# Performance work log

Hardware: AMD Instinct MI355X
Metric: run time of the kernel (lower is better)

## Reference

```python
import jax, jax.numpy as jnp
import numpy as np

B, N, S, D = 8, 325, 64, 256
H = 8
HD = D // H  # head_dim = 32


def setup_inputs() -> dict:
    key = jax.random.key(0)
    ks = jax.random.split(key, 5)
    x = jax.random.normal(ks[0], (B, N, S, D), dtype=jnp.float32)
    # nn.Linear params: weight [out, in], bias [out]
    w_qkv = jax.random.normal(ks[1], (3 * D, D), dtype=jnp.float32) * (1.0 / np.sqrt(D))
    b_qkv = jax.random.normal(ks[2], (3 * D,), dtype=jnp.float32) * 0.01
    w_proj = jax.random.normal(ks[3], (D, D), dtype=jnp.float32) * (1.0 / np.sqrt(D))
    b_proj = jax.random.normal(ks[4], (D,), dtype=jnp.float32) * 0.01
    return {"x": x, "w_qkv": w_qkv, "b_qkv": b_qkv, "w_proj": w_proj, "b_proj": b_proj}


def reference(x, w_qkv, b_qkv, w_proj, b_proj):
    b, n, s, d = x.shape
    scale = (d // H) ** -0.5
    xf = x.reshape(b * n, s, d)                              # [BN, S, D]
    qkv = jnp.einsum('bsd,ed->bse', xf, w_qkv) + b_qkv       # [BN, S, 3D]
    qkv = qkv.reshape(b * n, s, 3, H, HD)
    qkv = jnp.transpose(qkv, (2, 0, 3, 1, 4))                # [3, BN, H, S, HD]
    q, k, v = qkv[0], qkv[1], qkv[2]
    attn = jnp.einsum('bhqe,bhke->bhqk', q, k) * scale       # [BN, H, S, S]
    attn = jax.nn.softmax(attn, axis=-1)
    out = jnp.einsum('bhqk,bhke->bhqe', attn, v)             # [BN, H, S, HD]
    out = jnp.transpose(out, (0, 2, 1, 3)).reshape(b * n, s, d)
    out = jnp.einsum('bsd,ed->bse', out, w_proj) + b_proj
    return out.reshape(b, n, s, d)
```

## Files before the change

kernel.cpp:

```cpp
#include <hip/hip_runtime.h>
#include <hip/hip_bf16.h>


namespace {

constexpr int S_LEN = 64;
constexpr int DM    = 256;
constexpr int SD    = S_LEN * DM;
constexpr int NQKV  = 3 * DM * DM;

typedef float f32x4 __attribute__((ext_vector_type(4)));
typedef short s16x8 __attribute__((ext_vector_type(8)));

union BF2 { __hip_bfloat162 h; unsigned u; };
__device__ __forceinline__ unsigned pkbf2(float a, float b) {
  float2 t; t.x = a; t.y = b;
  BF2 cv; cv.h = __float22bfloat162_rn(t);
  return cv.u;
}

__device__ __forceinline__ s16x8 xpose_frag(f32x4 a0, f32x4 a1, int c, int g) {
  const int src0 = ((g & 1) << 5) + c;
  const int src1 = src0 + 16;
  unsigned p00 = pkbf2(a0[0], a0[1]);
  unsigned p01 = pkbf2(a0[2], a0[3]);
  unsigned p10 = pkbf2(a1[0], a1[1]);
  unsigned p11 = pkbf2(a1[2], a1[3]);
  const bool hi = (g & 2) != 0;
  unsigned w0a = (unsigned)__shfl((int)p00, src0);
  unsigned w0b = (unsigned)__shfl((int)p10, src0);
  unsigned w1a = (unsigned)__shfl((int)p01, src0);
  unsigned w1b = (unsigned)__shfl((int)p11, src0);
  unsigned w2a = (unsigned)__shfl((int)p00, src1);
  unsigned w2b = (unsigned)__shfl((int)p10, src1);
  unsigned w3a = (unsigned)__shfl((int)p01, src1);
  unsigned w3b = (unsigned)__shfl((int)p11, src1);
  union { s16x8 v; unsigned u[4]; } r;
  r.u[0] = hi ? w0b : w0a;
  r.u[1] = hi ? w1b : w1a;
  r.u[2] = hi ? w2b : w2a;
  r.u[3] = hi ? w3b : w3a;
  return r.v;
}

__device__ __forceinline__ int wswz(int row, int g) {
  return row * 32 + ((g ^ ((row >> 1) & 3)) << 3);
}

}

__global__ void ta_prep_weights(const float* __restrict__ wqkv,
                                const float* __restrict__ wproj,
                                unsigned short* __restrict__ wsb) {
  const int i = (blockIdx.x * 256 + (int)threadIdx.x) * 4;
  f32x4 v = (i < NQKV) ? *(const f32x4*)(wqkv + i)
                       : *(const f32x4*)(wproj + (i - NQKV));
  unsigned u0 = pkbf2(v[0], v[1]);
  unsigned u1 = pkbf2(v[2], v[3]);
  *(uint2*)(wsb + i) = make_uint2(u0, u1);
}

__global__ void __launch_bounds__(512, 1)
ta_fused_kernel(const float* __restrict__ x,
                const unsigned short* __restrict__ wq_bf,
                const float* __restrict__ bqkv,
                const unsigned short* __restrict__ wp_bf,
                const float* __restrict__ bproj,
                float* __restrict__ out)
{
  __shared__ __align__(16) unsigned short lds[65536];

  const int bn = blockIdx.x;
  const int tid = (int)threadIdx.x;
  const int w = tid >> 6;
  const int l = tid & 63;
  const int g = l >> 4;
  const int c = l & 15;
  const int c7s = (c & 7) << 3;
  const int h = w;

  unsigned short* __restrict__ xls = lds;
  unsigned short* wbuf[2] = { lds + 16384, lds + 40960 };

  const float* __restrict__ xb = x + (size_t)bn * SD;

  s16x8 wst[6];
#pragma unroll
  for (int i = 0; i < 6; ++i) {
    const int idx = i * 512 + tid, row = idx >> 2, gl = idx & 3;
    wst[i] = *(const s16x8*)&wq_bf[row * 256 + 0 * 32 + gl * 8];
  }

#pragma unroll
  for (int it = 0; it < 4; ++it) {
    const int e = (it * 512 + tid) * 8;
    const int row = e >> 8;
    f32x4 a = *(const f32x4*)(xb + e);
    f32x4 b = *(const f32x4*)(xb + e + 4);
    union { s16x8 v; unsigned u[4]; } r;
    r.u[0] = pkbf2(a[0], a[1]); r.u[1] = pkbf2(a[2], a[3]);
    r.u[2] = pkbf2(b[0], b[1]); r.u[3] = pkbf2(b[2], b[3]);
    *(s16x8*)&xls[e ^ ((row & 7) << 3)] = r.v;
  }
  __syncthreads();

#pragma unroll
  for (int i = 0; i < 6; ++i) {
    const int idx = i * 512 + tid, row = idx >> 2, gl = idx & 3;
    *(s16x8*)&wbuf[0][wswz(row, gl)] = wst[i];
  }
#pragma unroll
  for (int i = 0; i < 6; ++i) {
    const int idx = i * 512 + tid, row = idx >> 2, gl = idx & 3;
    wst[i] = *(const s16x8*)&wq_bf[row * 256 + 1 * 32 + gl * 8];
  }
  __syncthreads();

  f32x4 aq[2][4], ak[2][4], av[4][2];
#pragma unroll
  for (int t = 0; t < 2; ++t)
#pragma unroll
    for (int nj = 0; nj < 4; ++nj) {
      aq[t][nj] = f32x4{0.f, 0.f, 0.f, 0.f};
      ak[t][nj] = f32x4{0.f, 0.f, 0.f, 0.f};
    }
#pragma unroll
  for (int mt = 0; mt < 4; ++mt)
#pragma unroll
    for (int t = 0; t < 2; ++t) av[mt][t] = f32x4{0.f, 0.f, 0.f, 0.f};

#pragma unroll
  for (int ks = 0; ks < 8; ++ks) {
    const unsigned short* wb = wbuf[ks & 1];
    const int kof = ks * 32 + g * 8;
    s16x8 bx[4];
#pragma unroll
    for (int nj = 0; nj < 4; ++nj) {
      const int row = 16 * nj + c;
      bx[nj] = *(const s16x8*)&xls[(row * 256 + kof) ^ c7s];
    }
#pragma unroll
    for (int t = 0; t < 2; ++t) {
      s16x8 awq = *(const s16x8*)&wb[wswz((2 * h + t) * 16 + c, g)];
      s16x8 awk = *(const s16x8*)&wb[wswz(256 + 32 * h + 16 * t + c, g)];
      s16x8 awv = *(const s16x8*)&wb[wswz(512 + 32 * h + 16 * t + c, g)];
#pragma unroll
      for (int nj = 0; nj < 4; ++nj) {
        aq[t][nj] = __builtin_amdgcn_mfma_f32_16x16x32_bf16(awq, bx[nj], aq[t][nj], 0, 0, 0);
        ak[t][nj] = __builtin_amdgcn_mfma_f32_16x16x32_bf16(awk, bx[nj], ak[t][nj], 0, 0, 0);
        av[nj][t] = __builtin_amdgcn_mfma_f32_16x16x32_bf16(bx[nj], awv, av[nj][t], 0, 0, 0);
      }
    }
    if (ks < 7) {
#pragma unroll
      for (int i = 0; i < 6; ++i) {
        const int idx = i * 512 + tid, row = idx >> 2, gl = idx & 3;
        *(s16x8*)&wbuf[(ks + 1) & 1][wswz(row, gl)] = wst[i];
      }
    }
    if (ks < 6) {
#pragma unroll
      for (int i = 0; i < 6; ++i) {
        const int idx = i * 512 + tid, row = idx >> 2, gl = idx & 3;
        wst[i] = *(const s16x8*)&wq_bf[row * 256 + (ks + 2) * 32 + gl * 8];
      }
    }
    __syncthreads();
  }

  s16x8 pst[2];
#pragma unroll
  for (int i = 0; i < 2; ++i) {
    const int idx = i * 512 + tid, row = idx >> 2, gl = idx & 3;
    pst[i] = *(const s16x8*)&wp_bf[row * 256 + 0 * 32 + gl * 8];
  }

#pragma unroll
  for (int t = 0; t < 2; ++t) {
    f32x4 bq = *(const f32x4*)(bqkv + (2 * h + t) * 16 + 4 * g);
    f32x4 bk = *(const f32x4*)(bqkv + 256 + 32 * h + 16 * t + 4 * g);
#pragma unroll
    for (int nj = 0; nj < 4; ++nj) {
      aq[t][nj] += bq;
      ak[t][nj] += bk;
    }
  }
  {
    const float bv0 = bqkv[512 + 32 * h + c];
    const float bv1 = bqkv[512 + 32 * h + 16 + c];
#pragma unroll
    for (int mt = 0; mt < 4; ++mt)
#pragma unroll
      for (int r = 0; r < 4; ++r) {
        av[mt][0][r] += bv0;
        av[mt][1][r] += bv1;
      }
  }

  s16x8 qa[4], ka[4];
#pragma unroll
  for (int i = 0; i < 4; ++i) {
    qa[i] = xpose_frag(aq[0][i], aq[1][i], c, g);
    ka[i] = xpose_frag(ak[0][i], ak[1][i], c, g);
  }

  f32x4 sa[4][4];
#pragma unroll
  for (int ki = 0; ki < 4; ++ki)
#pragma unroll
    for (int qi = 0; qi < 4; ++qi) {
      f32x4 z = f32x4{0.f, 0.f, 0.f, 0.f};
      sa[ki][qi] = __builtin_amdgcn_mfma_f32_16x16x32_bf16(ka[ki], qa[qi], z, 0, 0, 0);
    }

  const float sc = 0.17677669529663687f * 1.4426950408889634f;
  float inv[4];
#pragma unroll
  for (int qi = 0; qi < 4; ++qi) {
    float m = sa[0][qi][0];
#pragma unroll
    for (int ki = 0; ki < 4; ++ki)
#pragma unroll
      for (int r = 0; r < 4; ++r) m = fmaxf(m, sa[ki][qi][r]);
    m = fmaxf(m, __shfl_xor(m, 16));
    m = fmaxf(m, __shfl_xor(m, 32));
    float s = 0.0f;
#pragma unroll
    for (int ki = 0; ki < 4; ++ki)
#pragma unroll
      for (int r = 0; r < 4; ++r) {
        float pv = exp2f((sa[ki][qi][r] - m) * sc);
        sa[ki][qi][r] = pv;
        s += pv;
      }
    s += __shfl_xor(s, 16);
    s += __shfl_xor(s, 32);
    inv[qi] = 1.0f / s;
  }

  s16x8 pa[4][2];
#pragma unroll
  for (int mi = 0; mi < 4; ++mi) {
    const float iv = inv[mi];
#pragma unroll
    for (int ks2 = 0; ks2 < 2; ++ks2) {
      f32x4 v0 = sa[2 * ks2][mi] * iv;
      f32x4 v1 = sa[2 * ks2 + 1][mi] * iv;
      pa[mi][ks2] = xpose_frag(v0, v1, c, g);
    }
  }

  s16x8 vb[2][2];
#pragma unroll
  for (int nd = 0; nd < 2; ++nd)
#pragma unroll
    for (int ks2 = 0; ks2 < 2; ++ks2)
      vb[nd][ks2] = xpose_frag(av[2 * ks2][nd], av[2 * ks2 + 1][nd], c, g);

  f32x4 oa[4][2];
#pragma unroll
  for (int mi = 0; mi < 4; ++mi)
#pragma unroll
    for (int nd = 0; nd < 2; ++nd) oa[mi][nd] = f32x4{0.f, 0.f, 0.f, 0.f};
#pragma unroll
  for (int ks2 = 0; ks2 < 2; ++ks2)
#pragma unroll
    for (int mi = 0; mi < 4; ++mi)
#pragma unroll
      for (int nd = 0; nd < 2; ++nd)
        oa[mi][nd] = __builtin_amdgcn_mfma_f32_16x16x32_bf16(pa[mi][ks2], vb[nd][ks2], oa[mi][nd], 0, 0, 0);

  unsigned obp[4][2][2];
#pragma unroll
  for (int mi = 0; mi < 4; ++mi)
#pragma unroll
    for (int nd = 0; nd < 2; ++nd) {
      obp[mi][nd][0] = pkbf2(oa[mi][nd][0], oa[mi][nd][1]);
      obp[mi][nd][1] = pkbf2(oa[mi][nd][2], oa[mi][nd][3]);
    }

#pragma unroll
  for (int mi = 0; mi < 4; ++mi)
#pragma unroll
    for (int nd = 0; nd < 2; ++nd)
#pragma unroll
      for (int r = 0; r < 4; ++r) {
        const int q = 16 * mi + 4 * g + r;
        const int feat = h * 32 + 16 * nd + c;
        unsigned val = obp[mi][nd][r >> 1] >> (16 * (r & 1));
        xls[(q * 256 + feat) ^ ((q & 7) << 3)] = (unsigned short)val;
      }
#pragma unroll
  for (int i = 0; i < 2; ++i) {
    const int idx = i * 512 + tid, row = idx >> 2, gl = idx & 3;
    *(s16x8*)&wbuf[0][wswz(row, gl)] = pst[i];
  }
#pragma unroll
  for (int i = 0; i < 2; ++i) {
    const int idx = i * 512 + tid, row = idx >> 2, gl = idx & 3;
    pst[i] = *(const s16x8*)&wp_bf[row * 256 + 1 * 32 + gl * 8];
  }
  __syncthreads();

  f32x4 pacc[2][4];
#pragma unroll
  for (int ti = 0; ti < 2; ++ti)
#pragma unroll
    for (int nj = 0; nj < 4; ++nj) pacc[ti][nj] = f32x4{0.f, 0.f, 0.f, 0.f};

#pragma unroll
  for (int ks = 0; ks < 8; ++ks) {
    const unsigned short* wb = wbuf[ks & 1];
    const int kof = ks * 32 + 8 * g;
    s16x8 bx[4];
#pragma unroll
    for (int nj = 0; nj < 4; ++nj) {
      const int row = 16 * nj + c;
      bx[nj] = *(const s16x8*)&xls[(row * 256 + kof) ^ c7s];
    }
#pragma unroll
    for (int ti = 0; ti < 2; ++ti) {
      s16x8 aw = *(const s16x8*)&wb[wswz((2 * w + ti) * 16 + c, g)];
#pragma unroll
      for (int nj = 0; nj < 4; ++nj)
        pacc[ti][nj] = __builtin_amdgcn_mfma_f32_16x16x32_bf16(aw, bx[nj], pacc[ti][nj], 0, 0, 0);
    }
    if (ks < 7) {
#pragma unroll
      for (int i = 0; i < 2; ++i) {
        const int idx = i * 512 + tid, row = idx >> 2, gl = idx & 3;
        *(s16x8*)&wbuf[(ks + 1) & 1][wswz(row, gl)] = pst[i];
      }
    }
    if (ks < 6) {
#pragma unroll
      for (int i = 0; i < 2; ++i) {
        const int idx = i * 512 + tid, row = idx >> 2, gl = idx & 3;
        pst[i] = *(const s16x8*)&wp_bf[row * 256 + (ks + 2) * 32 + gl * 8];
      }
    }
    __syncthreads();
  }

  float* ldsf = (float*)wbuf[0];
  float* __restrict__ ob = out + (size_t)bn * SD;
#pragma unroll
  for (int H = 0; H < 2; ++H) {
#pragma unroll
    for (int ti = 0; ti < 2; ++ti) {
      const int e0 = (2 * w + ti) * 16 + 4 * g;
      f32x4 bp = *(const f32x4*)(bproj + e0);
#pragma unroll
      for (int nj = 2 * H; nj < 2 * H + 2; ++nj) {
        const int lr = 16 * (nj - 2 * H) + c;
        f32x4 v;
        v[0] = pacc[ti][nj][0] + bp[0];
        v[1] = pacc[ti][nj][1] + bp[1];
        v[2] = pacc[ti][nj][2] + bp[2];
        v[3] = pacc[ti][nj][3] + bp[3];
        *(f32x4*)&ldsf[(lr * 256 + e0) ^ ((lr & 7) << 2)] = v;
      }
    }
    __syncthreads();
#pragma unroll
    for (int it = 0; it < 4; ++it) {
      const int i = (it * 512 + tid) * 4;
      const int lr = i >> 8;
      f32x4 v = *(const f32x4*)&ldsf[i ^ ((lr & 7) << 2)];
      *(f32x4*)(ob + H * 8192 + i) = v;
    }
    if (H == 0) __syncthreads();
  }
}

extern "C" void kernel_launch(void* const* d_in, const int* in_sizes, int n_in,
                              void* d_out, int out_size, void* d_ws, size_t ws_size,
                              hipStream_t stream) {
  (void)n_in; (void)ws_size; (void)out_size;
  const float* x     = (const float*)d_in[0];
  const float* wqkv  = (const float*)d_in[1];
  const float* bqkv  = (const float*)d_in[2];
  const float* wproj = (const float*)d_in[3];
  const float* bproj = (const float*)d_in[4];
  float* out = (float*)d_out;

  unsigned short* wsb = (unsigned short*)d_ws;
  const unsigned short* wq_bf = wsb;
  const unsigned short* wp_bf = wsb + NQKV;

  hipLaunchKernelGGL(ta_prep_weights, dim3(256), dim3(256), 0, stream, wqkv, wproj, wsb);

  const int bn_total = in_sizes[0] / SD;
  hipLaunchKernelGGL(ta_fused_kernel, dim3(bn_total), dim3(512), 0, stream,
                     x, wq_bf, bqkv, wp_bf, bproj, out);
}
```

Before: 243.9 us.

## Pre-tile weights per head so each wave streams a private LDS slice

The weight prep kernel now reorders the QKV and projection weights into per-head, per-k-step tiles. Each wave loads only its own 96x32 (QKV) or 32x32 (proj) slice into a private LDS region. This removes the block-wide barriers inside both K loops and shrinks shared memory from 128KB to 80KB. Launch bounds are raised to allow two blocks per CU, which caps registers at about 128 per thread and risks spilling given the large accumulator sets.

```diff
diff --git a/kernel.cpp b/kernel.cpp
--- a/kernel.cpp
+++ b/kernel.cpp
@@ -7,7 +7,8 @@
 constexpr int S_LEN = 64;
 constexpr int DM    = 256;
 constexpr int SD    = S_LEN * DM;
-constexpr int NQKV  = 3 * DM * DM;
+constexpr int NWQT  = 8 * 8 * 96 * 32;
+constexpr int NWPT  = 8 * 8 * 32 * 32;
 
 typedef float f32x4 __attribute__((ext_vector_type(4)));
 typedef short s16x8 __attribute__((ext_vector_type(8)));
@@ -43,8 +44,8 @@
   return r.v;
 }
 
-__device__ __forceinline__ int wswz(int row, int g) {
-  return row * 32 + ((g ^ ((row >> 1) & 3)) << 3);
+__device__ __forceinline__ int wswz(int row, int u) {
+  return row * 32 + ((u ^ ((row >> 1) & 3)) << 3);
 }
 
 }
@@ -52,23 +53,47 @@
 __global__ void ta_prep_weights(const float* __restrict__ wqkv,
                                 const float* __restrict__ wproj,
                                 unsigned short* __restrict__ wsb) {
-  const int i = (blockIdx.x * 256 + (int)threadIdx.x) * 4;
-  f32x4 v = (i < NQKV) ? *(const f32x4*)(wqkv + i)
-                       : *(const f32x4*)(wproj + (i - NQKV));
-  unsigned u0 = pkbf2(v[0], v[1]);
-  unsigned u1 = pkbf2(v[2], v[3]);
-  *(uint2*)(wsb + i) = make_uint2(u0, u1);
-}
-
-__global__ void __launch_bounds__(512, 1)
+  const int o = (blockIdx.x * 256 + (int)threadIdx.x) * 8;
+  const float* src;
+  if (o < NWQT) {
+    const int col = o & 31;
+    const int rf  = o >> 5;
+    const int j   = rf % 96;
+    const int t2  = rf / 96;
+    const int h   = t2 & 7;
+    const int ks  = t2 >> 3;
+    const int row = (j < 32) ? (32 * h + j)
+                  : (j < 64) ? (256 + 32 * h + (j - 32))
+                             : (512 + 32 * h + (j - 64));
+    src = wqkv + row * 256 + ks * 32 + col;
+  } else {
+    const int p   = o - NWQT;
+    const int col = p & 31;
+    const int rf  = p >> 5;
+    const int r   = rf & 31;
+    const int t2  = rf >> 5;
+    const int wv  = t2 & 7;
+    const int ks  = t2 >> 3;
+    src = wproj + (32 * wv + r) * 256 + ks * 32 + col;
+  }
+  f32x4 a = *(const f32x4*)src;
+  f32x4 b = *(const f32x4*)(src + 4);
+  unsigned u0 = pkbf2(a[0], a[1]);
+  unsigned u1 = pkbf2(a[2], a[3]);
+  unsigned u2 = pkbf2(b[0], b[1]);
+  unsigned u3 = pkbf2(b[2], b[3]);
+  *(uint4*)(wsb + o) = make_uint4(u0, u1, u2, u3);
+}
+
+__global__ void __launch_bounds__(512, 2)
 ta_fused_kernel(const float* __restrict__ x,
-                const unsigned short* __restrict__ wq_bf,
+                const unsigned short* __restrict__ wqt,
                 const float* __restrict__ bqkv,
-                const unsigned short* __restrict__ wp_bf,
+                const unsigned short* __restrict__ wpt,
                 const float* __restrict__ bproj,
                 float* __restrict__ out)
 {
-  __shared__ __align__(16) unsigned short lds[65536];
+  __shared__ __align__(16) unsigned short lds[40960];
 
   const int bn = blockIdx.x;
   const int tid = (int)threadIdx.x;
@@ -80,15 +105,18 @@
   const int h = w;
 
   unsigned short* __restrict__ xls = lds;
-  unsigned short* wbuf[2] = { lds + 16384, lds + 40960 };
+  unsigned short* __restrict__ wl  = lds + 16384 + w * 3072;
 
   const float* __restrict__ xb = x + (size_t)bn * SD;
 
+  const int sj = (0 * 64 + l) >> 2;
+  (void)sj;
+
   s16x8 wst[6];
 #pragma unroll
   for (int i = 0; i < 6; ++i) {
-    const int idx = i * 512 + tid, row = idx >> 2, gl = idx & 3;
-    wst[i] = *(const s16x8*)&wq_bf[row * 256 + 0 * 32 + gl * 8];
+    const int idx = i * 64 + l, j = idx >> 2, gl = idx & 3;
+    wst[i] = *(const s16x8*)&wqt[(0 * 8 + h) * 3072 + j * 32 + gl * 8];
   }
 
 #pragma unroll
@@ -106,15 +134,14 @@
 
 #pragma unroll
   for (int i = 0; i < 6; ++i) {
-    const int idx = i * 512 + tid, row = idx >> 2, gl = idx & 3;
-    *(s16x8*)&wbuf[0][wswz(row, gl)] = wst[i];
+    const int idx = i * 64 + l, j = idx >> 2, gl = idx & 3;
+    *(s16x8*)&wl[wswz(j, gl)] = wst[i];
   }
 #pragma unroll
   for (int i = 0; i < 6; ++i) {
-    const int idx = i * 512 + tid, row = idx >> 2, gl = idx & 3;
-    wst[i] = *(const s16x8*)&wq_bf[row * 256 + 1 * 32 + gl * 8];
-  }
-  __syncthreads();
+    const int idx = i * 64 + l, j = idx >> 2, gl = idx & 3;
+    wst[i] = *(const s16x8*)&wqt[(1 * 8 + h) * 3072 + j * 32 + gl * 8];
+  }
 
   f32x4 aq[2][4], ak[2][4], av[4][2];
 #pragma unroll
@@ -131,7 +158,6 @@
 
 #pragma unroll
   for (int ks = 0; ks < 8; ++ks) {
-    const unsigned short* wb = wbuf[ks & 1];
     const int kof = ks * 32 + g * 8;
     s16x8 bx[4];
 #pragma unroll
@@ -141,9 +167,9 @@
     }
 #pragma unroll
     for (int t = 0; t < 2; ++t) {
-      s16x8 awq = *(const s16x8*)&wb[wswz((2 * h + t) * 16 + c, g)];
-      s16x8 awk = *(const s16x8*)&wb[wswz(256 + 32 * h + 16 * t + c, g)];
-      s16x8 awv = *(const s16x8*)&wb[wswz(512 + 32 * h + 16 * t + c, g)];
+      s16x8 awq = *(const s16x8*)&wl[wswz(16 * t + c, g)];
+      s16x8 awk = *(const s16x8*)&wl[wswz(32 + 16 * t + c, g)];
+      s16x8 awv = *(const s16x8*)&wl[wswz(64 + 16 * t + c, g)];
 #pragma unroll
       for (int nj = 0; nj < 4; ++nj) {
         aq[t][nj] = __builtin_amdgcn_mfma_f32_16x16x32_bf16(awq, bx[nj], aq[t][nj], 0, 0, 0);
@@ -154,25 +180,17 @@
     if (ks < 7) {
 #pragma unroll
       for (int i = 0; i < 6; ++i) {
-        const int idx = i * 512 + tid, row = idx >> 2, gl = idx & 3;
-        *(s16x8*)&wbuf[(ks + 1) & 1][wswz(row, gl)] = wst[i];
+        const int idx = i * 64 + l, j = idx >> 2, gl = idx & 3;
+        *(s16x8*)&wl[wswz(j, gl)] = wst[i];
       }
     }
     if (ks < 6) {
 #pragma unroll
       for (int i = 0; i < 6; ++i) {
-        const int idx = i * 512 + tid, row = idx >> 2, gl = idx & 3;
-        wst[i] = *(const s16x8*)&wq_bf[row * 256 + (ks + 2) * 32 + gl * 8];
-      }
-    }
-    __syncthreads();
-  }
-
-  s16x8 pst[2];
-#pragma unroll
-  for (int i = 0; i < 2; ++i) {
-    const int idx = i * 512 + tid, row = idx >> 2, gl = idx & 3;
-    pst[i] = *(const s16x8*)&wp_bf[row * 256 + 0 * 32 + gl * 8];
+        const int idx = i * 64 + l, j = idx >> 2, gl = idx & 3;
+        wst[i] = *(const s16x8*)&wqt[((ks + 2) * 8 + h) * 3072 + j * 32 + gl * 8];
+      }
+    }
   }
 
 #pragma unroll
@@ -278,6 +296,8 @@
       obp[mi][nd][0] = pkbf2(oa[mi][nd][0], oa[mi][nd][1]);
       obp[mi][nd][1] = pkbf2(oa[mi][nd][2], oa[mi][nd][3]);
     }
+
+  __syncthreads();
 
 #pragma unroll
   for (int mi = 0; mi < 4; ++mi)
@@ -290,17 +310,24 @@
         unsigned val = obp[mi][nd][r >> 1] >> (16 * (r & 1));
         xls[(q * 256 + feat) ^ ((q & 7) << 3)] = (unsigned short)val;
       }
+  s16x8 pst[2];
 #pragma unroll
   for (int i = 0; i < 2; ++i) {
-    const int idx = i * 512 + tid, row = idx >> 2, gl = idx & 3;
-    *(s16x8*)&wbuf[0][wswz(row, gl)] = pst[i];
-  }
+    const int idx = i * 64 + l, r = idx >> 2, gl = idx & 3;
+    pst[i] = *(const s16x8*)&wpt[(0 * 8 + w) * 1024 + r * 32 + gl * 8];
+  }
+  __syncthreads();
+
 #pragma unroll
   for (int i = 0; i < 2; ++i) {
-    const int idx = i * 512 + tid, row = idx >> 2, gl = idx & 3;
-    pst[i] = *(const s16x8*)&wp_bf[row * 256 + 1 * 32 + gl * 8];
-  }
-  __syncthreads();
+    const int idx = i * 64 + l, r = idx >> 2, gl = idx & 3;
+    *(s16x8*)&wl[wswz(r, gl)] = pst[i];
+  }
+#pragma unroll
+  for (int i = 0; i < 2; ++i) {
+    const int idx = i * 64 + l, r = idx >> 2, gl = idx & 3;
+    pst[i] = *(const s16x8*)&wpt[(1 * 8 + w) * 1024 + r * 32 + gl * 8];
+  }
 
   f32x4 pacc[2][4];
 #pragma unroll
@@ -310,7 +337,6 @@
 
 #pragma unroll
   for (int ks = 0; ks < 8; ++ks) {
-    const unsigned short* wb = wbuf[ks & 1];
     const int kof = ks * 32 + 8 * g;
     s16x8 bx[4];
 #pragma unroll
@@ -320,7 +346,7 @@
     }
 #pragma unroll
     for (int ti = 0; ti < 2; ++ti) {
-      s16x8 aw = *(const s16x8*)&wb[wswz((2 * w + ti) * 16 + c, g)];
+      s16x8 aw = *(const s16x8*)&wl[wswz(16 * ti + c, g)];
 #pragma unroll
       for (int nj = 0; nj < 4; ++nj)
         pacc[ti][nj] = __builtin_amdgcn_mfma_f32_16x16x32_bf16(aw, bx[nj], pacc[ti][nj], 0, 0, 0);
@@ -328,21 +354,22 @@
     if (ks < 7) {
 #pragma unroll
       for (int i = 0; i < 2; ++i) {
-        const int idx = i * 512 + tid, row = idx >> 2, gl = idx & 3;
-        *(s16x8*)&wbuf[(ks + 1) & 1][wswz(row, gl)] = pst[i];
+        const int idx = i * 64 + l, r = idx >> 2, gl = idx & 3;
+        *(s16x8*)&wl[wswz(r, gl)] = pst[i];
       }
     }
     if (ks < 6) {
 #pragma unroll
       for (int i = 0; i < 2; ++i) {
-        const int idx = i * 512 + tid, row = idx >> 2, gl = idx & 3;
-        pst[i] = *(const s16x8*)&wp_bf[row * 256 + (ks + 2) * 32 + gl * 8];
-      }
-    }
-    __syncthreads();
-  }
-
-  float* ldsf = (float*)wbuf[0];
+        const int idx = i * 64 + l, r = idx >> 2, gl = idx & 3;
+        pst[i] = *(const s16x8*)&wpt[((ks + 2) * 8 + w) * 1024 + r * 32 + gl * 8];
+      }
+    }
+  }
+
+  __syncthreads();
+
+  float* ldsf = (float*)(lds + 16384);
   float* __restrict__ ob = out + (size_t)bn * SD;
 #pragma unroll
   for (int H = 0; H < 2; ++H) {
@@ -385,12 +412,12 @@
   float* out = (float*)d_out;
 
   unsigned short* wsb = (unsigned short*)d_ws;
-  const unsigned short* wq_bf = wsb;
-  const unsigned short* wp_bf = wsb + NQKV;
-
-  hipLaunchKernelGGL(ta_prep_weights, dim3(256), dim3(256), 0, stream, wqkv, wproj, wsb);
+  const unsigned short* wqt = wsb;
+  const unsigned short* wpt = wsb + NWQT;
+
+  hipLaunchKernelGGL(ta_prep_weights, dim3(128), dim3(256), 0, stream, wqkv, wproj, wsb);
 
   const int bn_total = in_sizes[0] / SD;
   hipLaunchKernelGGL(ta_fused_kernel, dim3(bn_total), dim3(512), 0, stream,
-                     x, wq_bf, bqkv, wp_bf, bproj, out);
-}
+                     x, wqt, bqkv, wpt, bproj, out);
+}
```

Result: slower. 266.7 us (+9.3%).
